# Performance work log

Hardware: AMD Instinct MI355X
Metric: run time of the kernel (lower is better)

## Reference

```python
import jax, jax.numpy as jnp
import numpy as np

PI = jnp.float32(3.14159265359)  # same truncated constant as the torch source
LOG_2PI = jnp.log(2.0 * PI)
STAB = 0.001  # covariance stabilizer added before inversion in the original


def _decoder(z, W1, b1, W2, b2, W3, b3, W4, b4):
    # f: Linear(z_dim,64)-ELU-Linear(64,128)-ELU-Linear(128,256)-ELU-Linear(256,784)-Sigmoid
    h = jax.nn.elu(z @ W1.T + b1)
    h = jax.nn.elu(h @ W2.T + b2)
    h = jax.nn.elu(h @ W3.T + b3)
    return jax.nn.sigmoid(h @ W4.T + b4)


def setup_inputs() -> dict:
    key = jax.random.key(0)
    ks = jax.random.split(key, 6)
    N, K, D, Z = 512, 256, 784, 2

    def lin(k, fan_in, fan_out):
        k1, k2 = jax.random.split(k)
        lim = 1.0 / np.sqrt(fan_in)
        W = jax.random.uniform(k1, (fan_out, fan_in), minval=-lim, maxval=lim, dtype=jnp.float32)
        b = jax.random.uniform(k2, (fan_out,), minval=-lim, maxval=lim, dtype=jnp.float32)
        return W, b

    W1, b1 = lin(ks[0], Z, 64)
    W2, b2 = lin(ks[1], 64, 128)
    W3, b3 = lin(ks[2], 128, 256)
    W4, b4 = lin(ks[3], 256, D)
    X = jax.random.uniform(ks[4], (N, D), dtype=jnp.float32)   # image pixels in [0,1)
    z = jax.random.normal(ks[5], (K, Z), dtype=jnp.float32)    # latent MC samples
    log_std = jnp.zeros((1,), dtype=jnp.float32)               # self.log_std_ = tensor([0.0])
    return dict(X=X, z=z, log_std=log_std, W1=W1, b1=b1, W2=W2, b2=b2,
                W3=W3, b3=b3, W4=W4, b4=b4)


def reference(X, z, log_std, W1, b1, W2, b2, W3, b3, W4, b4):
    # expected_log_likelihood(X, z) == objective(X, z, variational=False)
    N, D = X.shape
    K, Z = z.shape
    s = jnp.exp(log_std[0])  # isotropic likelihood variance (covariance = s * I_D)

    # --- log_likelihood: MVN log-prob with covariance s*I_D (closed form of det/inverse) ---
    params = _decoder(z, W1, b1, W2, b2, W3, b3, W4, b4)           # (K, D)
    diffs = X[:, None, :] - params[None, :, :]                      # (N, K, D) dominant traffic
    quad = jnp.sum(diffs * diffs, axis=-1) / (s + STAB)             # inv((s+eps)*I) = I/(s+eps)
    log_norm = -0.5 * D * LOG_2PI - 0.5 * (D * log_std[0])          # log det(s*I_D) = D*log s
    ll = log_norm - 0.5 * quad                                      # (N, K)

    # --- log_prior: MVN log-prob with identity covariance (stabilized inverse: I/1.001) ---
    log_prior = -0.5 * Z * LOG_2PI - 0.5 * jnp.sum(z * z, axis=-1) / (1.0 + STAB)  # (K,)

    # --- importance weights computed under no_grad in the original ---
    sg = jax.lax.stop_gradient
    ll_c = sg(ll)
    lp_c = sg(log_prior)
    m = jnp.max(ll_c)
    ll_s = ll_c - m                                                 # (N, K)
    log_joint_s = ll_s + lp_c[None, :]                              # (N, K)
    evidence_s = jnp.exp(ll_s).sum(axis=-1) / K                     # (N,)
    log_evidence_s = jnp.log(evidence_s)
    log_posteriors = (log_joint_s - log_evidence_s[:, None]).T      # (K, N)
    iw = jnp.exp(log_posteriors - lp_c[:, None])                    # (K, N), constants

    ell = (iw.T * ll).sum(axis=-1) / K                              # (N,)
    return ell.sum() / N
```

## Files before the change

### kernel.cpp

```cpp
#include <hip/hip_runtime.h>
#include <math.h>

#define LOG_2PI 1.8378770664093453f

__device__ __forceinline__ float elu_f(float x) {
    return x > 0.0f ? x : expm1f(x);
}
__device__ __forceinline__ float sigmoid_f(float x) {
    return 1.0f / (1.0f + expf(-x));
}

__global__ __launch_bounds__(256) void decoder_kernel(
    const float* __restrict__ z,
    const float* __restrict__ W1, const float* __restrict__ b1,
    const float* __restrict__ W2, const float* __restrict__ b2,
    const float* __restrict__ W3, const float* __restrict__ b3,
    const float* __restrict__ W4, const float* __restrict__ b4,
    float* __restrict__ PT)
{
    __shared__ __align__(16) float h1[4][64];
    __shared__ __align__(16) float h2[4][128];
    __shared__ __align__(16) float h3[4][256];

    const int t  = threadIdx.x;
    const int kt = blockIdx.x >> 1;
    const int jh = blockIdx.x & 1;
    const int k0 = kt * 4;

    {
        int kl = t >> 6, o = t & 63;
        float z0 = z[(k0 + kl) * 2 + 0];
        float z1 = z[(k0 + kl) * 2 + 1];
        float v = fmaf(z0, W1[o * 2 + 0], fmaf(z1, W1[o * 2 + 1], b1[o]));
        h1[kl][o] = elu_f(v);
    }
    __syncthreads();

    for (int idx = t; idx < 512; idx += 256) {
        int kl = idx >> 7, o = idx & 127;
        const float4* wr = reinterpret_cast<const float4*>(W2 + o * 64);
        const float4* hr = reinterpret_cast<const float4*>(h1[kl]);
        float acc = b2[o];
        #pragma unroll
        for (int i = 0; i < 16; ++i) {
            float4 w = wr[i]; float4 a = hr[i];
            acc = fmaf(w.x, a.x, acc); acc = fmaf(w.y, a.y, acc);
            acc = fmaf(w.z, a.z, acc); acc = fmaf(w.w, a.w, acc);
        }
        h2[kl][o] = elu_f(acc);
    }
    __syncthreads();

    for (int idx = t; idx < 1024; idx += 256) {
        int kl = idx >> 8, o = idx & 255;
        const float4* wr = reinterpret_cast<const float4*>(W3 + o * 128);
        const float4* hr = reinterpret_cast<const float4*>(h2[kl]);
        float acc = b3[o];
        #pragma unroll
        for (int i = 0; i < 32; ++i) {
            float4 w = wr[i]; float4 a = hr[i];
            acc = fmaf(w.x, a.x, acc); acc = fmaf(w.y, a.y, acc);
            acc = fmaf(w.z, a.z, acc); acc = fmaf(w.w, a.w, acc);
        }
        h3[kl][o] = elu_f(acc);
    }
    __syncthreads();

    const int jbeg = jh * 392, jend = jbeg + 392;
    for (int j = jbeg + t; j < jend; j += 256) {
        const float4* wr = reinterpret_cast<const float4*>(W4 + j * 256);
        const float4* h0 = reinterpret_cast<const float4*>(h3[0]);
        const float4* hA = reinterpret_cast<const float4*>(h3[1]);
        const float4* hB = reinterpret_cast<const float4*>(h3[2]);
        const float4* hC = reinterpret_cast<const float4*>(h3[3]);
        float bb = b4[j];
        float a0 = bb, a1 = bb, a2 = bb, a3 = bb;
        #pragma unroll 8
        for (int i = 0; i < 64; ++i) {
            float4 w = wr[i];
            float4 x0 = h0[i], x1 = hA[i], x2 = hB[i], x3 = hC[i];
            a0 = fmaf(w.x, x0.x, a0); a0 = fmaf(w.y, x0.y, a0);
            a0 = fmaf(w.z, x0.z, a0); a0 = fmaf(w.w, x0.w, a0);
            a1 = fmaf(w.x, x1.x, a1); a1 = fmaf(w.y, x1.y, a1);
            a1 = fmaf(w.z, x1.z, a1); a1 = fmaf(w.w, x1.w, a1);
            a2 = fmaf(w.x, x2.x, a2); a2 = fmaf(w.y, x2.y, a2);
            a2 = fmaf(w.z, x2.z, a2); a2 = fmaf(w.w, x2.w, a2);
            a3 = fmaf(w.x, x3.x, a3); a3 = fmaf(w.y, x3.y, a3);
            a3 = fmaf(w.z, x3.z, a3); a3 = fmaf(w.w, x3.w, a3);
        }
        float* row = PT + j * 256 + k0;
        row[0] = sigmoid_f(a0);
        row[1] = sigmoid_f(a1);
        row[2] = sigmoid_f(a2);
        row[3] = sigmoid_f(a3);
    }
}

__global__ __launch_bounds__(256) void quad_ell_kernel(
    const float* __restrict__ X, const float* __restrict__ log_std,
    const float* __restrict__ PT, float* __restrict__ ell)
{
    __shared__ __align__(16) float Xs[2][784];
    __shared__ __align__(16) float4 red[2][64];

    const int t  = threadIdx.x;
    const int n0 = blockIdx.x * 2;

    for (int d = t; d < 784; d += 256) {
        Xs[0][d] = X[n0 * 784 + d];
        Xs[1][d] = X[(n0 + 1) * 784 + d];
    }
    __syncthreads();

    const int w  = t >> 6, l = t & 63;
    const int nl = w >> 1, dh = w & 1;
    const float4* PT4 = reinterpret_cast<const float4*>(PT);

    float ax = 0.0f, ay = 0.0f, az = 0.0f, aw = 0.0f;
    const int dbeg = dh * 392, dend = dbeg + 392;
    #pragma unroll 4
    for (int d = dbeg; d < dend; ++d) {
        float4 p = PT4[d * 64 + l];
        float x = Xs[nl][d];
        float d0 = x - p.x, d1 = x - p.y, d2 = x - p.z, d3 = x - p.w;
        ax = fmaf(d0, d0, ax); ay = fmaf(d1, d1, ay);
        az = fmaf(d2, d2, az); aw = fmaf(d3, d3, aw);
    }

    if (dh == 1) red[nl][l] = make_float4(ax, ay, az, aw);
    __syncthreads();
    if (dh == 0) {
        float4 r = red[nl][l];
        ax += r.x; ay += r.y; az += r.z; aw += r.w;

        float ls  = log_std[0];
        float s   = expf(ls);
        float inv = 1.0f / (s + 0.001f);
        float log_norm = -0.5f * 784.0f * LOG_2PI - 0.5f * 784.0f * ls;

        float ll0 = log_norm - 0.5f * ax * inv;
        float ll1 = log_norm - 0.5f * ay * inv;
        float ll2 = log_norm - 0.5f * az * inv;
        float ll3 = log_norm - 0.5f * aw * inv;

        float m = fmaxf(fmaxf(ll0, ll1), fmaxf(ll2, ll3));
        for (int off = 32; off > 0; off >>= 1)
            m = fmaxf(m, __shfl_down(m, off));
        m = __shfl(m, 0);

        float e0 = expf(ll0 - m), e1 = expf(ll1 - m);
        float e2 = expf(ll2 - m), e3 = expf(ll3 - m);
        float s0 = (e0 + e1) + (e2 + e3);
        float s1 = fmaf(e0, ll0, fmaf(e1, ll1, fmaf(e2, ll2, e3 * ll3)));
        for (int off = 32; off > 0; off >>= 1) {
            s0 += __shfl_down(s0, off);
            s1 += __shfl_down(s1, off);
        }
        if (l == 0) ell[n0 + nl] = s1 / s0;
    }
}

__global__ __launch_bounds__(256) void finalize_kernel(
    const float* __restrict__ ell, float* __restrict__ out)
{
    __shared__ float part[4];
    const int t = threadIdx.x;
    float v = ell[t] + ell[t + 256];
    for (int off = 32; off > 0; off >>= 1)
        v += __shfl_down(v, off);
    if ((t & 63) == 0) part[t >> 6] = v;
    __syncthreads();
    if (t == 0)
        out[0] = (part[0] + part[1] + part[2] + part[3]) * (1.0f / 512.0f);
}

extern "C" void kernel_launch(void* const* d_in, const int* in_sizes, int n_in,
                              void* d_out, int out_size, void* d_ws, size_t ws_size,
                              hipStream_t stream) {
    const float* X       = (const float*)d_in[0];
    const float* z       = (const float*)d_in[1];
    const float* log_std = (const float*)d_in[2];
    const float* W1      = (const float*)d_in[3];
    const float* b1      = (const float*)d_in[4];
    const float* W2      = (const float*)d_in[5];
    const float* b2      = (const float*)d_in[6];
    const float* W3      = (const float*)d_in[7];
    const float* b3      = (const float*)d_in[8];
    const float* W4      = (const float*)d_in[9];
    const float* b4      = (const float*)d_in[10];
    float* out = (float*)d_out;

    float* wsf = (float*)d_ws;
    float* PT  = wsf;
    float* ell = wsf + 200704;

    decoder_kernel<<<128, 256, 0, stream>>>(z, W1, b1, W2, b2, W3, b3, W4, b4, PT);
    quad_ell_kernel<<<256, 256, 0, stream>>>(X, log_std, PT, ell);
    finalize_kernel<<<1, 256, 0, stream>>>(ell, out);
}
```

Baseline: 138.9 us.

## Retile quad kernel over 8 rows by K-quarters with split softmax merge

The decoder grid doubles to 256 blocks: each block handles one quarter of the output columns, and results are written as a single float4. The quad kernel now stages 8 X rows per block and splits K into four quarters across blocks. Each half-wave reduces its D halves through shuffles and writes partial (max, sum, weighted-sum) triples. Finalize merges those partials with a log-sum-exp style rescale, so the block-level shared-memory reduction is replaced by shuffles and each PT column segment is reused across more X rows. The cost is extra partial-output traffic and a heavier finalize step.

```diff
diff --git a/kernel.cpp b/kernel.cpp
--- a/kernel.cpp
+++ b/kernel.cpp
@@ -23,8 +23,8 @@
     __shared__ __align__(16) float h3[4][256];
 
     const int t  = threadIdx.x;
-    const int kt = blockIdx.x >> 1;
-    const int jh = blockIdx.x & 1;
+    const int kt = blockIdx.x >> 2;
+    const int jq = blockIdx.x & 3;
     const int k0 = kt * 4;
 
     {
@@ -66,8 +66,8 @@
     }
     __syncthreads();
 
-    const int jbeg = jh * 392, jend = jbeg + 392;
-    for (int j = jbeg + t; j < jend; j += 256) {
+    if (t < 196) {
+        const int j = jq * 196 + t;
         const float4* wr = reinterpret_cast<const float4*>(W4 + j * 256);
         const float4* h0 = reinterpret_cast<const float4*>(h3[0]);
         const float4* hA = reinterpret_cast<const float4*>(h3[1]);
@@ -88,90 +88,107 @@
             a3 = fmaf(w.x, x3.x, a3); a3 = fmaf(w.y, x3.y, a3);
             a3 = fmaf(w.z, x3.z, a3); a3 = fmaf(w.w, x3.w, a3);
         }
-        float* row = PT + j * 256 + k0;
-        row[0] = sigmoid_f(a0);
-        row[1] = sigmoid_f(a1);
-        row[2] = sigmoid_f(a2);
-        row[3] = sigmoid_f(a3);
-    }
-}
-
-__global__ __launch_bounds__(256) void quad_ell_kernel(
+        float4 r = make_float4(sigmoid_f(a0), sigmoid_f(a1),
+                               sigmoid_f(a2), sigmoid_f(a3));
+        *reinterpret_cast<float4*>(PT + j * 256 + k0) = r;
+    }
+}
+
+__global__ __launch_bounds__(256) void quad_part_kernel(
     const float* __restrict__ X, const float* __restrict__ log_std,
-    const float* __restrict__ PT, float* __restrict__ ell)
+    const float* __restrict__ PT, float* __restrict__ part)
 {
-    __shared__ __align__(16) float Xs[2][784];
-    __shared__ __align__(16) float4 red[2][64];
+    __shared__ __align__(16) float Xs[8 * 784];
 
     const int t  = threadIdx.x;
-    const int n0 = blockIdx.x * 2;
-
-    for (int d = t; d < 784; d += 256) {
-        Xs[0][d] = X[n0 * 784 + d];
-        Xs[1][d] = X[(n0 + 1) * 784 + d];
+    const int nb = blockIdx.x >> 2;
+    const int bq = blockIdx.x & 3;
+    const int n0 = nb * 8;
+
+    {
+        const float4* X4  = reinterpret_cast<const float4*>(X + n0 * 784);
+        float4*       Xs4 = reinterpret_cast<float4*>(Xs);
+        for (int i = t; i < 1568; i += 256) Xs4[i] = X4[i];
     }
     __syncthreads();
 
     const int w  = t >> 6, l = t & 63;
-    const int nl = w >> 1, dh = w & 1;
-    const float4* PT4 = reinterpret_cast<const float4*>(PT);
+    const int rl = 2 * w + (l >> 5);
+    const int dh = (l >> 4) & 1;
+    const int kv = l & 15;
+
+    const float4* P4   = reinterpret_cast<const float4*>(PT) + bq * 16 + kv;
+    const float*  xrow = Xs + rl * 784 + dh * 392;
+    const int     dofs = dh * 392;
 
     float ax = 0.0f, ay = 0.0f, az = 0.0f, aw = 0.0f;
-    const int dbeg = dh * 392, dend = dbeg + 392;
     #pragma unroll 4
-    for (int d = dbeg; d < dend; ++d) {
-        float4 p = PT4[d * 64 + l];
-        float x = Xs[nl][d];
+    for (int d = 0; d < 392; ++d) {
+        float4 p = P4[(dofs + d) * 64];
+        float x = xrow[d];
         float d0 = x - p.x, d1 = x - p.y, d2 = x - p.z, d3 = x - p.w;
         ax = fmaf(d0, d0, ax); ay = fmaf(d1, d1, ay);
         az = fmaf(d2, d2, az); aw = fmaf(d3, d3, aw);
     }
 
-    if (dh == 1) red[nl][l] = make_float4(ax, ay, az, aw);
-    __syncthreads();
-    if (dh == 0) {
-        float4 r = red[nl][l];
-        ax += r.x; ay += r.y; az += r.z; aw += r.w;
-
-        float ls  = log_std[0];
-        float s   = expf(ls);
-        float inv = 1.0f / (s + 0.001f);
-        float log_norm = -0.5f * 784.0f * LOG_2PI - 0.5f * 784.0f * ls;
-
-        float ll0 = log_norm - 0.5f * ax * inv;
-        float ll1 = log_norm - 0.5f * ay * inv;
-        float ll2 = log_norm - 0.5f * az * inv;
-        float ll3 = log_norm - 0.5f * aw * inv;
-
-        float m = fmaxf(fmaxf(ll0, ll1), fmaxf(ll2, ll3));
-        for (int off = 32; off > 0; off >>= 1)
-            m = fmaxf(m, __shfl_down(m, off));
-        m = __shfl(m, 0);
-
-        float e0 = expf(ll0 - m), e1 = expf(ll1 - m);
-        float e2 = expf(ll2 - m), e3 = expf(ll3 - m);
-        float s0 = (e0 + e1) + (e2 + e3);
-        float s1 = fmaf(e0, ll0, fmaf(e1, ll1, fmaf(e2, ll2, e3 * ll3)));
-        for (int off = 32; off > 0; off >>= 1) {
-            s0 += __shfl_down(s0, off);
-            s1 += __shfl_down(s1, off);
-        }
-        if (l == 0) ell[n0 + nl] = s1 / s0;
+    ax += __shfl_xor(ax, 16); ay += __shfl_xor(ay, 16);
+    az += __shfl_xor(az, 16); aw += __shfl_xor(aw, 16);
+
+    float ls  = log_std[0];
+    float s   = expf(ls);
+    float inv = 1.0f / (s + 0.001f);
+    float log_norm = -0.5f * 784.0f * LOG_2PI - 0.5f * 784.0f * ls;
+
+    float ll0 = log_norm - 0.5f * ax * inv;
+    float ll1 = log_norm - 0.5f * ay * inv;
+    float ll2 = log_norm - 0.5f * az * inv;
+    float ll3 = log_norm - 0.5f * aw * inv;
+
+    float m = fmaxf(fmaxf(ll0, ll1), fmaxf(ll2, ll3));
+    for (int off = 1; off < 16; off <<= 1)
+        m = fmaxf(m, __shfl_xor(m, off));
+
+    float e0 = expf(ll0 - m), e1 = expf(ll1 - m);
+    float e2 = expf(ll2 - m), e3 = expf(ll3 - m);
+    float s0 = (e0 + e1) + (e2 + e3);
+    float s1 = fmaf(e0, ll0, fmaf(e1, ll1, fmaf(e2, ll2, e3 * ll3)));
+    for (int off = 1; off < 16; off <<= 1) {
+        s0 += __shfl_xor(s0, off);
+        s1 += __shfl_xor(s1, off);
+    }
+
+    if ((l & 31) == 0) {
+        int row = n0 + rl;
+        float* pp = part + (row * 4 + bq) * 3;
+        pp[0] = m; pp[1] = s0; pp[2] = s1;
     }
 }
 
 __global__ __launch_bounds__(256) void finalize_kernel(
-    const float* __restrict__ ell, float* __restrict__ out)
+    const float* __restrict__ part, float* __restrict__ out)
 {
-    __shared__ float part[4];
+    __shared__ float red[4];
     const int t = threadIdx.x;
-    float v = ell[t] + ell[t + 256];
+    float v = 0.0f;
+    #pragma unroll
+    for (int h = 0; h < 2; ++h) {
+        const float* pp = part + (t + h * 256) * 12;
+        float M = fmaxf(fmaxf(pp[0], pp[3]), fmaxf(pp[6], pp[9]));
+        float S0 = 0.0f, S1 = 0.0f;
+        #pragma unroll
+        for (int q = 0; q < 4; ++q) {
+            float f = expf(pp[q * 3] - M);
+            S0 = fmaf(pp[q * 3 + 1], f, S0);
+            S1 = fmaf(pp[q * 3 + 2], f, S1);
+        }
+        v += S1 / S0;
+    }
     for (int off = 32; off > 0; off >>= 1)
         v += __shfl_down(v, off);
-    if ((t & 63) == 0) part[t >> 6] = v;
+    if ((t & 63) == 0) red[t >> 6] = v;
     __syncthreads();
     if (t == 0)
-        out[0] = (part[0] + part[1] + part[2] + part[3]) * (1.0f / 512.0f);
+        out[0] = (red[0] + red[1] + red[2] + red[3]) * (1.0f / 512.0f);
 }
 
 extern "C" void kernel_launch(void* const* d_in, const int* in_sizes, int n_in,
@@ -190,11 +207,11 @@
     const float* b4      = (const float*)d_in[10];
     float* out = (float*)d_out;
 
-    float* wsf = (float*)d_ws;
-    float* PT  = wsf;
-    float* ell = wsf + 200704;
-
-    decoder_kernel<<<128, 256, 0, stream>>>(z, W1, b1, W2, b2, W3, b3, W4, b4, PT);
-    quad_ell_kernel<<<256, 256, 0, stream>>>(X, log_std, PT, ell);
-    finalize_kernel<<<1, 256, 0, stream>>>(ell, out);
-}
+    float* wsf  = (float*)d_ws;
+    float* PT   = wsf;
+    float* part = wsf + 200704;
+
+    decoder_kernel<<<256, 256, 0, stream>>>(z, W1, b1, W2, b2, W3, b3, W4, b4, PT);
+    quad_part_kernel<<<256, 256, 0, stream>>>(X, log_std, PT, part);
+    finalize_kernel<<<1, 256, 0, stream>>>(part, out);
+}
```

Measured after the change: 131.8 us. 5.2% less time.
